# Kernel tuning notes

Hardware: AMD Instinct MI355X
Metric: run time of the kernel (lower is better)

The kernel has to match this reference:

```python
import jax, jax.numpy as jnp
import numpy as np

B, T, C = 2, 2048, 768
H, N_LEFT = 12, 6
D = C // H


def setup_inputs() -> dict:
    key = jax.random.key(0)
    ks = jax.random.split(key, 4)
    x = jax.random.normal(ks[0], (B, T, C), dtype=jnp.float32)
    attention_mask = jnp.ones((B, T), dtype=jnp.int32)
    Wqkv_w = jax.random.normal(ks[1], (3 * C, C), dtype=jnp.float32) * (C ** -0.5)
    Wqkv_b = jnp.zeros((3 * C,), dtype=jnp.float32)
    Wo_w = jax.random.normal(ks[2], (C, C), dtype=jnp.float32) * (C ** -0.5)
    Wo_b = jnp.zeros((C,), dtype=jnp.float32)
    return {"x": x, "attention_mask": attention_mask, "Wqkv_w": Wqkv_w,
            "Wqkv_b": Wqkv_b, "Wo_w": Wo_w, "Wo_b": Wo_b}


def _attend(q, k, v, mask):
    # q,k,v: [B,h,T,D]; mask: [B,1,T,T] additive
    s = jnp.einsum('bhqd,bhkd->bhqk', q, k) * (D ** -0.5) + mask
    a = jax.nn.softmax(s.astype(jnp.float32), axis=-1).astype(q.dtype)
    return jnp.einsum('bhqk,bhkd->bhqd', a, v)


def reference(x, attention_mask, Wqkv_w, Wqkv_b, Wo_w, Wo_b):
    neg = jnp.finfo(x.dtype).min
    # padding mask [B,1,1,T]: 0 where valid, neg where padded
    pad = (1.0 - attention_mask.astype(x.dtype))[:, None, None, :] * neg
    i = jnp.arange(T)
    tri = (i[None, :] > i[:, None]).astype(x.dtype) * neg   # triu(neg, 1)
    left_mask = tri[None, None] + pad                        # causal (look left)
    right_mask = tri.T[None, None] + pad                     # anti-causal (look right)

    qkv = (x @ Wqkv_w.T + Wqkv_b).reshape(B, T, 3, H, D)
    qkv = jnp.transpose(qkv, (0, 3, 2, 1, 4))                # [B,H,3,T,D]
    q, k, v = qkv[:, :, 0], qkv[:, :, 1], qkv[:, :, 2]

    lc = _attend(q[:, :N_LEFT], k[:, :N_LEFT], v[:, :N_LEFT], left_mask)
    rc = _attend(q[:, N_LEFT:], k[:, N_LEFT:], v[:, N_LEFT:], right_mask)
    ctx = jnp.concatenate([lc, rc], axis=1)                  # [B,H,T,D]
    ctx = jnp.transpose(ctx, (0, 2, 1, 3)).reshape(B, T, C)
    out = ctx @ Wo_w.T + Wo_b
    return out
```

## Files before the change

kernel.cpp:

```cpp
#include <hip/hip_runtime.h>


typedef unsigned short u16;
typedef __bf16 bf16x8 __attribute__((ext_vector_type(8)));
typedef float fx4 __attribute__((ext_vector_type(4)));
typedef unsigned short u16x8 __attribute__((ext_vector_type(8)));
typedef unsigned short u16x4 __attribute__((ext_vector_type(4)));
typedef _Float16 hx4 __attribute__((ext_vector_type(4)));
typedef __fp16 fp16x2 __attribute__((ext_vector_type(2)));

#define T_SEQ 2048
#define C_DIM 768
#define NHEAD 12
#define HDIM  64
#define NITEMS 768
#define LOG2E_8 0.18033688f

__device__ __forceinline__ u16 f2bf(float f) {
  unsigned u = __float_as_uint(f);
  u += 0x7fffu + ((u >> 16) & 1u);
  return (u16)(u >> 16);
}
__device__ __forceinline__ u16 f2h(float f) {
  union { _Float16 h; u16 u; } cv; cv.h = (_Float16)f; return cv.u;
}

__device__ __forceinline__ void gl2lds16(const u16* g, u16* l) {
  __builtin_amdgcn_global_load_lds(
      (const __attribute__((address_space(1))) void*)g,
      (__attribute__((address_space(3))) void*)l, 16, 0, 0);
}

__global__ void cvt_swz_k(const float* __restrict__ in, u16* __restrict__ out, int n8) {
  int i = blockIdx.x * blockDim.x + threadIdx.x;
  if (i >= n8) return;
  const fx4* p = (const fx4*)in + (size_t)i * 2;
  fx4 a = p[0], b = p[1];
  u16x8 o;
  #pragma unroll
  for (int j = 0; j < 4; ++j) { o[j] = f2bf(a[j]); o[4 + j] = f2bf(b[j]); }
  int m = i / 96;
  int c8 = (i - m * 96) << 3;
  *(u16x8*)&out[(size_t)m * C_DIM + (c8 ^ ((m & 7) << 3))] = o;
}

__global__ void maskcvt_k(const int* __restrict__ am, float* __restrict__ mf, int n) {
  int i = blockIdx.x * blockDim.x + threadIdx.x;
  if (i < n) mf[i] = am[i] ? 0.f : -1e30f;
}

__device__ __forceinline__ void gemm_core128(const u16* __restrict__ A,
                                             const u16* __restrict__ B,
                                             int m0, int n0,
                                             u16* As, u16* Bs,
                                             fx4 acc[4][4]) {
  const int tid = threadIdx.x;
  const int lane = tid & 63, wv = tid >> 6;
  const int wm = (wv & 1) << 6, wn = (wv >> 1) << 6;
  const int lr = lane & 15, lg = lane >> 4;
  const int swk = (lr & 7) << 3;
  const int srow = (wv << 3) + (lane >> 3);
  const int scol = (lane & 7) << 3;
  #pragma unroll
  for (int mt = 0; mt < 4; ++mt)
    #pragma unroll
    for (int nt = 0; nt < 4; ++nt) acc[mt][nt] = fx4{0.f, 0.f, 0.f, 0.f};

  #pragma unroll
  for (int p = 0; p < 4; ++p) {
    int row = srow + (p << 5);
    gl2lds16(&A[(size_t)(m0 + row) * C_DIM + scol], &As[(row << 6) + scol]);
    gl2lds16(&B[(size_t)(n0 + row) * C_DIM + scol], &Bs[(row << 6) + scol]);
  }

  int buf = 0;
  for (int k0 = 0; k0 < C_DIM; k0 += 64, buf ^= 1) {
    __syncthreads();
    if (k0 + 64 < C_DIM) {
      u16* Ad = &As[(buf ^ 1) << 13];
      u16* Bd = &Bs[(buf ^ 1) << 13];
      #pragma unroll
      for (int p = 0; p < 4; ++p) {
        int row = srow + (p << 5);
        gl2lds16(&A[(size_t)(m0 + row) * C_DIM + k0 + 64 + scol], &Ad[(row << 6) + scol]);
        gl2lds16(&B[(size_t)(n0 + row) * C_DIM + k0 + 64 + scol], &Bd[(row << 6) + scol]);
      }
    }
    const u16* Ab = &As[buf << 13];
    const u16* Bb = &Bs[buf << 13];
    #pragma unroll
    for (int kk = 0; kk < 64; kk += 32) {
      bf16x8 af[4], bfr[4];
      #pragma unroll
      for (int mt = 0; mt < 4; ++mt)
        af[mt] = *(const bf16x8*)&Ab[((wm + mt * 16 + lr) << 6) + ((kk + lg * 8) ^ swk)];
      #pragma unroll
      for (int nt = 0; nt < 4; ++nt)
        bfr[nt] = *(const bf16x8*)&Bb[((wn + nt * 16 + lr) << 6) + ((kk + lg * 8) ^ swk)];
      #pragma unroll
      for (int mt = 0; mt < 4; ++mt)
        #pragma unroll
        for (int nt = 0; nt < 4; ++nt)
          acc[mt][nt] = __builtin_amdgcn_mfma_f32_16x16x32_bf16(
              af[mt], bfr[nt], acc[mt][nt], 0, 0, 0);
    }
  }
}

__global__ __launch_bounds__(256) void gemm_qkv_k(
    const u16* __restrict__ A, const u16* __restrict__ B,
    const float* __restrict__ bias,
    u16* __restrict__ qb, u16* __restrict__ kswz, u16* __restrict__ vswz) {
  __shared__ __align__(16) u16 As[2][128 * 64];
  __shared__ __align__(16) u16 Bs[2][128 * 64];
  int m0 = blockIdx.y << 7, n0 = blockIdx.x << 7;
  fx4 acc[4][4];
  gemm_core128(A, B, m0, n0, &As[0][0], &Bs[0][0], acc);

  const int tid = threadIdx.x, lane = tid & 63, wv = tid >> 6;
  const int wm = (wv & 1) << 6, wn = (wv >> 1) << 6;
  const int lr = lane & 15, lg = lane >> 4;
  #pragma unroll
  for (int nt = 0; nt < 4; ++nt) {
    int n = n0 + wn + nt * 16 + lr;
    float bv = bias[n];
    int part = n / 768;
    int rem = n - part * 768;
    int h = rem >> 6, d = rem & 63;
    #pragma unroll
    for (int mt = 0; mt < 4; ++mt) {
      #pragma unroll
      for (int r = 0; r < 4; ++r) {
        int m = m0 + wm + mt * 16 + lg * 4 + r;
        int bb = m >> 11, t = m & 2047;
        int bh = bb * NHEAD + h;
        int kt = t >> 6, tr = t & 63;
        float val = acc[mt][nt][r] + bv;
        if (part == 0) {
          qb[(((size_t)bh << 11) + t) * HDIM + d] = f2bf(val);
        } else if (part == 1) {
          kswz[((size_t)(bh * 32 + kt) << 12) + (tr << 6) + (d ^ ((tr & 7) << 3))] =
              f2bf(val);
        } else {
          vswz[((size_t)(bh * 32 + kt) << 12) + (d << 6) + (tr ^ ((d & 15) << 2))] =
              f2h(val);
        }
      }
    }
  }
}

__device__ __forceinline__ void gemm_core64(const u16* __restrict__ A,
                                            const u16* __restrict__ B,
                                            int m0, int n0,
                                            u16* As, u16* Bs,
                                            fx4 acc[4][2]) {
  const int tid = threadIdx.x;
  const int lane = tid & 63, wv = tid >> 6;
  const int wn = wv << 5;
  const int lr = lane & 15, lg = lane >> 4;
  const int swk = (lr & 7) << 3;
  const int srow = (wv << 3) + (lane >> 3);
  const int scol = (lane & 7) << 3;
  #pragma unroll
  for (int mt = 0; mt < 4; ++mt)
    #pragma unroll
    for (int nt = 0; nt < 2; ++nt) acc[mt][nt] = fx4{0.f, 0.f, 0.f, 0.f};

  #pragma unroll
  for (int p = 0; p < 2; ++p) {
    int row = srow + (p << 5);
    gl2lds16(&A[(size_t)(m0 + row) * C_DIM + scol], &As[(row << 6) + scol]);
  }
  #pragma unroll
  for (int p = 0; p < 4; ++p) {
    int row = srow + (p << 5);
    gl2lds16(&B[(size_t)(n0 + row) * C_DIM + scol], &Bs[(row << 6) + scol]);
  }

  int buf = 0;
  for (int k0 = 0; k0 < C_DIM; k0 += 64, buf ^= 1) {
    __syncthreads();
    if (k0 + 64 < C_DIM) {
      u16* Ad = &As[(buf ^ 1) << 12];
      u16* Bd = &Bs[(buf ^ 1) << 13];
      #pragma unroll
      for (int p = 0; p < 2; ++p) {
        int row = srow + (p << 5);
        gl2lds16(&A[(size_t)(m0 + row) * C_DIM + k0 + 64 + scol], &Ad[(row << 6) + scol]);
      }
      #pragma unroll
      for (int p = 0; p < 4; ++p) {
        int row = srow + (p << 5);
        gl2lds16(&B[(size_t)(n0 + row) * C_DIM + k0 + 64 + scol], &Bd[(row << 6) + scol]);
      }
    }
    const u16* Ab = &As[buf << 12];
    const u16* Bb = &Bs[buf << 13];
    #pragma unroll
    for (int kk = 0; kk < 64; kk += 32) {
      bf16x8 af[4], bfr[2];
      #pragma unroll
      for (int mt = 0; mt < 4; ++mt)
        af[mt] = *(const bf16x8*)&Ab[((mt * 16 + lr) << 6) + ((kk + lg * 8) ^ swk)];
      #pragma unroll
      for (int nt = 0; nt < 2; ++nt)
        bfr[nt] = *(const bf16x8*)&Bb[((wn + nt * 16 + lr) << 6) + ((kk + lg * 8) ^ swk)];
      #pragma unroll
      for (int mt = 0; mt < 4; ++mt)
        #pragma unroll
        for (int nt = 0; nt < 2; ++nt)
          acc[mt][nt] = __builtin_amdgcn_mfma_f32_16x16x32_bf16(
              af[mt], bfr[nt], acc[mt][nt], 0, 0, 0);
    }
  }
}

__global__ __launch_bounds__(256) void gemm_out_k(
    const u16* __restrict__ A, const u16* __restrict__ B,
    const float* __restrict__ bias, float* __restrict__ out) {
  __shared__ __align__(16) u16 As[2][64 * 64];
  __shared__ __align__(16) u16 Bs[2][128 * 64];
  int m0 = blockIdx.y << 6, n0 = blockIdx.x << 7;
  fx4 acc[4][2];
  gemm_core64(A, B, m0, n0, &As[0][0], &Bs[0][0], acc);

  const int tid = threadIdx.x, lane = tid & 63, wv = tid >> 6;
  const int wn = wv << 5;
  const int lr = lane & 15, lg = lane >> 4;
  #pragma unroll
  for (int nt = 0; nt < 2; ++nt) {
    int n = n0 + wn + nt * 16 + lr;
    float bv = bias[n];
    #pragma unroll
    for (int mt = 0; mt < 4; ++mt) {
      #pragma unroll
      for (int r = 0; r < 4; ++r) {
        int m = m0 + mt * 16 + lg * 4 + r;
        out[(size_t)m * C_DIM + n] = acc[mt][nt][r] + bv;
      }
    }
  }
}

__global__ __launch_bounds__(256) void attn_k(
    const u16* __restrict__ q, const u16* __restrict__ kswz,
    const u16* __restrict__ vswz, const float* __restrict__ maskf,
    u16* __restrict__ ctx, int* __restrict__ counter) {
  __shared__ __align__(16) u16 Ks[2][4096];
  __shared__ __align__(16) u16 Vt[2][4096];
  __shared__ int s_w;

  const int tid = threadIdx.x, lane = tid & 63, wv = tid >> 6;
  const int lr = lane & 15, lg = lane >> 4;
  const int swk = (lr & 7) << 3;
  const int swv = (lr & 15) << 2;

  for (;;) {
    if (tid == 0) s_w = atomicAdd(counter, 1);
    __syncthreads();
    int w = s_w;
    if (w >= NITEMS) break;
    int qslot = w / 24, bh = w - qslot * 24;
    int bb = bh / NHEAD, h = bh - bb * NHEAD;
    bool causal = (h < 6);
    int qt = causal ? (31 - qslot) : qslot;
    int kt0 = causal ? 0 : qt;
    int kt1 = causal ? qt : 31;
    size_t tile_base = (size_t)(bh * 32) << 12;

    {
      const u16* kg = kswz + tile_base + ((size_t)kt0 << 12);
      const u16* vg = vswz + tile_base + ((size_t)kt0 << 12);
      #pragma unroll
      for (int c2 = 0; c2 < 2; ++c2) {
        int e = (wv << 10) + (c2 << 9) + (lane << 3);
        gl2lds16(kg + e, &Ks[0][e]);
        gl2lds16(vg + e, &Vt[0][e]);
      }
    }

    int q0 = qt << 6;
    size_t head_off = ((size_t)bh << 11) * HDIM;
    int qrow = q0 + wv * 16 + lr;
    bf16x8 qf0 = *(const bf16x8*)&q[head_off + (size_t)qrow * HDIM + lg * 8];
    bf16x8 qf1 = *(const bf16x8*)&q[head_off + (size_t)qrow * HDIM + 32 + lg * 8];
    const float* mrow = maskf + (bb << 11);

    fx4 o[4];
    #pragma unroll
    for (int dt = 0; dt < 4; ++dt) o[dt] = fx4{0.f, 0.f, 0.f, 0.f};
    float l_i = 0.f;

    int buf = 0;
    for (int kt = kt0; kt <= kt1; ++kt, buf ^= 1) {
      __syncthreads();
      if (kt < kt1) {
        const u16* kg = kswz + tile_base + ((size_t)(kt + 1) << 12);
        const u16* vg = vswz + tile_base + ((size_t)(kt + 1) << 12);
        #pragma unroll
        for (int c2 = 0; c2 < 2; ++c2) {
          int e = (wv << 10) + (c2 << 9) + (lane << 3);
          gl2lds16(kg + e, &Ks[buf ^ 1][e]);
          gl2lds16(vg + e, &Vt[buf ^ 1][e]);
        }
      }

      fx4 st[4];
      #pragma unroll
      for (int nt = 0; nt < 4; ++nt) {
        const u16* kr = &Ks[buf][(nt * 16 + lr) << 6];
        bf16x8 kf0 = *(const bf16x8*)&kr[(lg * 8) ^ swk];
        bf16x8 kf1 = *(const bf16x8*)&kr[(32 + lg * 8) ^ swk];
        fx4 z = fx4{0.f, 0.f, 0.f, 0.f};
        z = __builtin_amdgcn_mfma_f32_16x16x32_bf16(kf0, qf0, z, 0, 0, 0);
        st[nt] = __builtin_amdgcn_mfma_f32_16x16x32_bf16(kf1, qf1, z, 0, 0, 0);
      }

      const bool diag = (kt == qt);
      float psum = 0.f;
      #pragma unroll
      for (int nt = 0; nt < 4; ++nt) {
        int kb0 = (kt << 6) + nt * 16 + lg * 4;
        fx4 mv = *(const fx4*)&mrow[kb0];
        #pragma unroll
        for (int r = 0; r < 4; ++r) {
          float arg = st[nt][r] * LOG2E_8 + mv[r];
          if (diag) {
            int kabs = kb0 + r;
            bool dead = causal ? (kabs > qrow) : (kabs < qrow);
            arg = dead ? -1e30f : arg;
          }
          float p = __builtin_amdgcn_exp2f(arg);
          st[nt][r] = p;
          psum += p;
        }
      }
      l_i += psum;

      #pragma unroll
      for (int nt = 0; nt < 4; ++nt) {
        union { hx4 v; fp16x2 h[2]; } pu;
        pu.h[0] = __builtin_amdgcn_cvt_pkrtz(st[nt][0], st[nt][1]);
        pu.h[1] = __builtin_amdgcn_cvt_pkrtz(st[nt][2], st[nt][3]);
        hx4 pf = pu.v;
        #pragma unroll
        for (int dt = 0; dt < 4; ++dt) {
          const u16* vr = &Vt[buf][(dt * 16 + lr) << 6];
          hx4 vf = *(const hx4*)&vr[(nt * 16 + lg * 4) ^ swv];
          o[dt] = __builtin_amdgcn_mfma_f32_16x16x16f16(vf, pf, o[dt], 0, 0, 0);
        }
      }
    }

    l_i += __shfl_xor(l_i, 16, 64);
    l_i += __shfl_xor(l_i, 32, 64);
    float inv = 1.f / l_i;
    size_t rowb = ((size_t)(bb << 11) + qrow) * C_DIM;
    int csw = (qrow & 7) << 3;
    #pragma unroll
    for (int dt = 0; dt < 4; ++dt) {
      u16x4 pk;
      #pragma unroll
      for (int r = 0; r < 4; ++r) pk[r] = f2bf(o[dt][r] * inv);
      int colb = h * HDIM + dt * 16 + lg * 4;
      *(u16x4*)&ctx[rowb + (colb ^ csw)] = pk;
    }
  }
}

extern "C" void kernel_launch(void* const* d_in, const int* in_sizes, int n_in,
                              void* d_out, int out_size, void* d_ws, size_t ws_size,
                              hipStream_t stream) {
  const float* x     = (const float*)d_in[0];
  const int*   amask = (const int*)d_in[1];
  const float* wqkv  = (const float*)d_in[2];
  const float* bqkv  = (const float*)d_in[3];
  const float* wo    = (const float*)d_in[4];
  const float* bo    = (const float*)d_in[5];
  float* out = (float*)d_out;

  char* ws = (char*)d_ws;
  u16*   xb    = (u16*)(ws + 0);
  u16*   wqkvb = (u16*)(ws + 6291456);
  u16*   wob   = (u16*)(ws + 9830400);
  u16*   qb    = (u16*)(ws + 11010048);
  u16*   kswz  = (u16*)(ws + 17301504);
  u16*   vswz  = (u16*)(ws + 23592960);
  u16*   ctxb  = (u16*)(ws + 29884416);
  float* maskf = (float*)(ws + 36175872);
  int*   cnt   = (int*)(ws + 36192256);

  cvt_swz_k<<<(393216 + 255) / 256, 256, 0, stream>>>(x, xb, 393216);
  cvt_swz_k<<<(221184 + 255) / 256, 256, 0, stream>>>(wqkv, wqkvb, 221184);
  cvt_swz_k<<<(73728 + 255) / 256, 256, 0, stream>>>(wo, wob, 73728);
  maskcvt_k<<<16, 256, 0, stream>>>(amask, maskf, 4096);
  (void)hipMemsetAsync(cnt, 0, 4, stream);

  gemm_qkv_k<<<dim3(18, 32), 256, 0, stream>>>(xb, wqkvb, bqkv, qb, kswz, vswz);
  attn_k<<<512, 256, 0, stream>>>(qb, kswz, vswz, maskf, ctxb, cnt);
  gemm_out_k<<<dim3(6, 64), 256, 0, stream>>>(ctxb, wob, bo, out);
}
```

Before: 189.4 us.

## Merge conversion launches, shrink GEMM K-tile to 32, raise attention grid size

The three fp32-to-bf16 conversion launches become one kernel that picks its source tensor by row index. It relies on the workspace buffers for x, Wqkv and Wo being contiguous. Both GEMM cores now stage 32-wide K tiles instead of 64, with a new LDS swizzle that keeps the global source layout intact. This halves shared memory per block but doubles the number of barriers per GEMM. The attention launch grows from 512 to 640 blocks, presumably to improve occupancy or load balance through its atomic work counter.

After: 207.0 us. +9.3%, slower.

```diff
diff --git a/kernel.cpp b/kernel.cpp
--- a/kernel.cpp
+++ b/kernel.cpp
@@ -31,16 +31,22 @@
       (__attribute__((address_space(3))) void*)l, 16, 0, 0);
 }
 
-__global__ void cvt_swz_k(const float* __restrict__ in, u16* __restrict__ out, int n8) {
+__global__ void cvt_swz_k(const float* __restrict__ x,
+                          const float* __restrict__ wqkv,
+                          const float* __restrict__ wo,
+                          u16* __restrict__ out) {
   int i = blockIdx.x * blockDim.x + threadIdx.x;
-  if (i >= n8) return;
-  const fx4* p = (const fx4*)in + (size_t)i * 2;
-  fx4 a = p[0], b = p[1];
-  u16x8 o;
-  #pragma unroll
-  for (int j = 0; j < 4; ++j) { o[j] = f2bf(a[j]); o[4 + j] = f2bf(b[j]); }
+  if (i >= 688128) return;
   int m = i / 96;
   int c8 = (i - m * 96) << 3;
+  const float* src;
+  if (m < 4096)       src = x    + (size_t)m * C_DIM + c8;
+  else if (m < 6400)  src = wqkv + (size_t)(m - 4096) * C_DIM + c8;
+  else                src = wo   + (size_t)(m - 6400) * C_DIM + c8;
+  fx4 a = *(const fx4*)src, b = *(const fx4*)(src + 4);
+  u16x8 o;
+  #pragma unroll
+  for (int j = 0; j < 4; ++j) { o[j] = f2bf(a[j]); o[4 + j] = f2bf(b[j]); }
   *(u16x8*)&out[(size_t)m * C_DIM + (c8 ^ ((m & 7) << 3))] = o;
 }
 
@@ -58,52 +64,60 @@
   const int lane = tid & 63, wv = tid >> 6;
   const int wm = (wv & 1) << 6, wn = (wv >> 1) << 6;
   const int lr = lane & 15, lg = lane >> 4;
-  const int swk = (lr & 7) << 3;
-  const int srow = (wv << 3) + (lane >> 3);
-  const int scol = (lane & 7) << 3;
   #pragma unroll
   for (int mt = 0; mt < 4; ++mt)
     #pragma unroll
     for (int nt = 0; nt < 4; ++nt) acc[mt][nt] = fx4{0.f, 0.f, 0.f, 0.f};
 
-  #pragma unroll
-  for (int p = 0; p < 4; ++p) {
-    int row = srow + (p << 5);
-    gl2lds16(&A[(size_t)(m0 + row) * C_DIM + scol], &As[(row << 6) + scol]);
-    gl2lds16(&B[(size_t)(n0 + row) * C_DIM + scol], &Bs[(row << 6) + scol]);
+  int srow[2], sgc[2];
+  #pragma unroll
+  for (int p = 0; p < 2; ++p) {
+    int c = tid + (p << 8);
+    srow[p] = c >> 2;
+    sgc[p] = c & 3;
+  }
+
+  #pragma unroll
+  for (int p = 0; p < 2; ++p) {
+    int row = srow[p];
+    int gcol = ((sgc[p] ^ (row & 3)) << 3) ^ ((row & 7) << 3);
+    gl2lds16(&A[(size_t)(m0 + row) * C_DIM + gcol], &As[(tid + (p << 8)) << 3]);
+    gl2lds16(&B[(size_t)(n0 + row) * C_DIM + gcol], &Bs[(tid + (p << 8)) << 3]);
   }
 
   int buf = 0;
-  for (int k0 = 0; k0 < C_DIM; k0 += 64, buf ^= 1) {
+  for (int k0 = 0; k0 < C_DIM; k0 += 32, buf ^= 1) {
     __syncthreads();
-    if (k0 + 64 < C_DIM) {
-      u16* Ad = &As[(buf ^ 1) << 13];
-      u16* Bd = &Bs[(buf ^ 1) << 13];
-      #pragma unroll
-      for (int p = 0; p < 4; ++p) {
-        int row = srow + (p << 5);
-        gl2lds16(&A[(size_t)(m0 + row) * C_DIM + k0 + 64 + scol], &Ad[(row << 6) + scol]);
-        gl2lds16(&B[(size_t)(n0 + row) * C_DIM + k0 + 64 + scol], &Bd[(row << 6) + scol]);
-      }
-    }
-    const u16* Ab = &As[buf << 13];
-    const u16* Bb = &Bs[buf << 13];
-    #pragma unroll
-    for (int kk = 0; kk < 64; kk += 32) {
-      bf16x8 af[4], bfr[4];
-      #pragma unroll
-      for (int mt = 0; mt < 4; ++mt)
-        af[mt] = *(const bf16x8*)&Ab[((wm + mt * 16 + lr) << 6) + ((kk + lg * 8) ^ swk)];
+    if (k0 + 32 < C_DIM) {
+      u16* Ad = &As[(buf ^ 1) << 12];
+      u16* Bd = &Bs[(buf ^ 1) << 12];
+      #pragma unroll
+      for (int p = 0; p < 2; ++p) {
+        int row = srow[p];
+        int gcol = (k0 + 32 + ((sgc[p] ^ (row & 3)) << 3)) ^ ((row & 7) << 3);
+        gl2lds16(&A[(size_t)(m0 + row) * C_DIM + gcol], &Ad[(tid + (p << 8)) << 3]);
+        gl2lds16(&B[(size_t)(n0 + row) * C_DIM + gcol], &Bd[(tid + (p << 8)) << 3]);
+      }
+    }
+    const u16* Ab = &As[buf << 12];
+    const u16* Bb = &Bs[buf << 12];
+    bf16x8 af[4], bfr[4];
+    #pragma unroll
+    for (int mt = 0; mt < 4; ++mt) {
+      int R = wm + mt * 16 + lr;
+      af[mt] = *(const bf16x8*)&Ab[(R << 5) + ((lg ^ (R & 3)) << 3)];
+    }
+    #pragma unroll
+    for (int nt = 0; nt < 4; ++nt) {
+      int R = wn + nt * 16 + lr;
+      bfr[nt] = *(const bf16x8*)&Bb[(R << 5) + ((lg ^ (R & 3)) << 3)];
+    }
+    #pragma unroll
+    for (int mt = 0; mt < 4; ++mt)
       #pragma unroll
       for (int nt = 0; nt < 4; ++nt)
-        bfr[nt] = *(const bf16x8*)&Bb[((wn + nt * 16 + lr) << 6) + ((kk + lg * 8) ^ swk)];
-      #pragma unroll
-      for (int mt = 0; mt < 4; ++mt)
-        #pragma unroll
-        for (int nt = 0; nt < 4; ++nt)
-          acc[mt][nt] = __builtin_amdgcn_mfma_f32_16x16x32_bf16(
-              af[mt], bfr[nt], acc[mt][nt], 0, 0, 0);
-    }
+        acc[mt][nt] = __builtin_amdgcn_mfma_f32_16x16x32_bf16(
+            af[mt], bfr[nt], acc[mt][nt], 0, 0, 0);
   }
 }
 
@@ -111,8 +125,8 @@
     const u16* __restrict__ A, const u16* __restrict__ B,
     const float* __restrict__ bias,
     u16* __restrict__ qb, u16* __restrict__ kswz, u16* __restrict__ vswz) {
-  __shared__ __align__(16) u16 As[2][128 * 64];
-  __shared__ __align__(16) u16 Bs[2][128 * 64];
+  __shared__ __align__(16) u16 As[2][128 * 32];
+  __shared__ __align__(16) u16 Bs[2][128 * 32];
   int m0 = blockIdx.y << 7, n0 = blockIdx.x << 7;
   fx4 acc[4][4];
   gemm_core128(A, B, m0, n0, &As[0][0], &Bs[0][0], acc);
@@ -159,68 +173,72 @@
   const int lane = tid & 63, wv = tid >> 6;
   const int wn = wv << 5;
   const int lr = lane & 15, lg = lane >> 4;
-  const int swk = (lr & 7) << 3;
-  const int srow = (wv << 3) + (lane >> 3);
-  const int scol = (lane & 7) << 3;
   #pragma unroll
   for (int mt = 0; mt < 4; ++mt)
     #pragma unroll
     for (int nt = 0; nt < 2; ++nt) acc[mt][nt] = fx4{0.f, 0.f, 0.f, 0.f};
 
+  int arow = tid >> 2, ac8 = tid & 3;
+  int brow[2], bc8[2];
   #pragma unroll
   for (int p = 0; p < 2; ++p) {
-    int row = srow + (p << 5);
-    gl2lds16(&A[(size_t)(m0 + row) * C_DIM + scol], &As[(row << 6) + scol]);
-  }
-  #pragma unroll
-  for (int p = 0; p < 4; ++p) {
-    int row = srow + (p << 5);
-    gl2lds16(&B[(size_t)(n0 + row) * C_DIM + scol], &Bs[(row << 6) + scol]);
+    int c = tid + (p << 8);
+    brow[p] = c >> 2; bc8[p] = c & 3;
+  }
+
+  {
+    int gcolA = ((ac8 ^ (arow & 3)) << 3) ^ ((arow & 7) << 3);
+    gl2lds16(&A[(size_t)(m0 + arow) * C_DIM + gcolA], &As[tid << 3]);
+    #pragma unroll
+    for (int p = 0; p < 2; ++p) {
+      int row = brow[p];
+      int gcol = ((bc8[p] ^ (row & 3)) << 3) ^ ((row & 7) << 3);
+      gl2lds16(&B[(size_t)(n0 + row) * C_DIM + gcol], &Bs[(tid + (p << 8)) << 3]);
+    }
   }
 
   int buf = 0;
-  for (int k0 = 0; k0 < C_DIM; k0 += 64, buf ^= 1) {
+  for (int k0 = 0; k0 < C_DIM; k0 += 32, buf ^= 1) {
     __syncthreads();
-    if (k0 + 64 < C_DIM) {
-      u16* Ad = &As[(buf ^ 1) << 12];
-      u16* Bd = &Bs[(buf ^ 1) << 13];
+    if (k0 + 32 < C_DIM) {
+      u16* Ad = &As[(buf ^ 1) << 11];
+      u16* Bd = &Bs[(buf ^ 1) << 12];
+      int gcolA = (k0 + 32 + ((ac8 ^ (arow & 3)) << 3)) ^ ((arow & 7) << 3);
+      gl2lds16(&A[(size_t)(m0 + arow) * C_DIM + gcolA], &Ad[tid << 3]);
       #pragma unroll
       for (int p = 0; p < 2; ++p) {
-        int row = srow + (p << 5);
-        gl2lds16(&A[(size_t)(m0 + row) * C_DIM + k0 + 64 + scol], &Ad[(row << 6) + scol]);
-      }
-      #pragma unroll
-      for (int p = 0; p < 4; ++p) {
-        int row = srow + (p << 5);
-        gl2lds16(&B[(size_t)(n0 + row) * C_DIM + k0 + 64 + scol], &Bd[(row << 6) + scol]);
-      }
-    }
-    const u16* Ab = &As[buf << 12];
-    const u16* Bb = &Bs[buf << 13];
-    #pragma unroll
-    for (int kk = 0; kk < 64; kk += 32) {
-      bf16x8 af[4], bfr[2];
-      #pragma unroll
-      for (int mt = 0; mt < 4; ++mt)
-        af[mt] = *(const bf16x8*)&Ab[((mt * 16 + lr) << 6) + ((kk + lg * 8) ^ swk)];
+        int row = brow[p];
+        int gcol = (k0 + 32 + ((bc8[p] ^ (row & 3)) << 3)) ^ ((row & 7) << 3);
+        gl2lds16(&B[(size_t)(n0 + row) * C_DIM + gcol], &Bd[(tid + (p << 8)) << 3]);
+      }
+    }
+    const u16* Ab = &As[buf << 11];
+    const u16* Bb = &Bs[buf << 12];
+    bf16x8 af[4], bfr[2];
+    #pragma unroll
+    for (int mt = 0; mt < 4; ++mt) {
+      int R = mt * 16 + lr;
+      af[mt] = *(const bf16x8*)&Ab[(R << 5) + ((lg ^ (R & 3)) << 3)];
+    }
+    #pragma unroll
+    for (int nt = 0; nt < 2; ++nt) {
+      int R = wn + nt * 16 + lr;
+      bfr[nt] = *(const bf16x8*)&Bb[(R << 5) + ((lg ^ (R & 3)) << 3)];
+    }
+    #pragma unroll
+    for (int mt = 0; mt < 4; ++mt)
       #pragma unroll
       for (int nt = 0; nt < 2; ++nt)
-        bfr[nt] = *(const bf16x8*)&Bb[((wn + nt * 16 + lr) << 6) + ((kk + lg * 8) ^ swk)];
-      #pragma unroll
-      for (int mt = 0; mt < 4; ++mt)
-        #pragma unroll
-        for (int nt = 0; nt < 2; ++nt)
-          acc[mt][nt] = __builtin_amdgcn_mfma_f32_16x16x32_bf16(
-              af[mt], bfr[nt], acc[mt][nt], 0, 0, 0);
-    }
+        acc[mt][nt] = __builtin_amdgcn_mfma_f32_16x16x32_bf16(
+            af[mt], bfr[nt], acc[mt][nt], 0, 0, 0);
   }
 }
 
 __global__ __launch_bounds__(256) void gemm_out_k(
     const u16* __restrict__ A, const u16* __restrict__ B,
     const float* __restrict__ bias, float* __restrict__ out) {
-  __shared__ __align__(16) u16 As[2][64 * 64];
-  __shared__ __align__(16) u16 Bs[2][128 * 64];
+  __shared__ __align__(16) u16 As[2][64 * 32];
+  __shared__ __align__(16) u16 Bs[2][128 * 32];
   int m0 = blockIdx.y << 6, n0 = blockIdx.x << 7;
   fx4 acc[4][2];
   gemm_core64(A, B, m0, n0, &As[0][0], &Bs[0][0], acc);
@@ -391,13 +409,11 @@
   float* maskf = (float*)(ws + 36175872);
   int*   cnt   = (int*)(ws + 36192256);
 
-  cvt_swz_k<<<(393216 + 255) / 256, 256, 0, stream>>>(x, xb, 393216);
-  cvt_swz_k<<<(221184 + 255) / 256, 256, 0, stream>>>(wqkv, wqkvb, 221184);
-  cvt_swz_k<<<(73728 + 255) / 256, 256, 0, stream>>>(wo, wob, 73728);
+  cvt_swz_k<<<2688, 256, 0, stream>>>(x, wqkv, wo, xb);
   maskcvt_k<<<16, 256, 0, stream>>>(amask, maskf, 4096);
   (void)hipMemsetAsync(cnt, 0, 4, stream);
 
   gemm_qkv_k<<<dim3(18, 32), 256, 0, stream>>>(xb, wqkvb, bqkv, qb, kswz, vswz);
-  attn_k<<<512, 256, 0, stream>>>(qb, kswz, vswz, maskf, ctxb, cnt);
+  attn_k<<<640, 256, 0, stream>>>(qb, kswz, vswz, maskf, ctxb, cnt);
   gemm_out_k<<<dim3(6, 64), 256, 0, stream>>>(ctxb, wob, bo, out);
 }
```

## Merge conversion launches, shrink GEMM tiles, split diagonal softmax path

Applied to the files above, without the earlier changes.

Combines the three fp32-to-bf16 conversion kernels into a single launch writing into the contiguous workspace. The QKV GEMM moves to 64x128 tiles and the output GEMM to 64x64 tiles, with single-buffered LDS loads and two barriers per k-step, raising block count for better CU occupancy. The attention softmax hoists the diagonal-tile check out of the inner loop so off-diagonal tiles skip masking logic. Dropping double buffering may expose global load latency.

Measured after the change: 170.7 us. -9.9%, faster.

```diff
diff --git a/kernel.cpp b/kernel.cpp
--- a/kernel.cpp
+++ b/kernel.cpp
@@ -31,16 +31,22 @@
       (__attribute__((address_space(3))) void*)l, 16, 0, 0);
 }
 
-__global__ void cvt_swz_k(const float* __restrict__ in, u16* __restrict__ out, int n8) {
+__global__ void cvt_swz_k(const float* __restrict__ x,
+                          const float* __restrict__ wqkv,
+                          const float* __restrict__ wo,
+                          u16* __restrict__ out) {
   int i = blockIdx.x * blockDim.x + threadIdx.x;
-  if (i >= n8) return;
-  const fx4* p = (const fx4*)in + (size_t)i * 2;
-  fx4 a = p[0], b = p[1];
-  u16x8 o;
-  #pragma unroll
-  for (int j = 0; j < 4; ++j) { o[j] = f2bf(a[j]); o[4 + j] = f2bf(b[j]); }
+  if (i >= 688128) return;
   int m = i / 96;
   int c8 = (i - m * 96) << 3;
+  const float* src;
+  if (m < 4096)       src = x    + (size_t)m * C_DIM + c8;
+  else if (m < 6400)  src = wqkv + (size_t)(m - 4096) * C_DIM + c8;
+  else                src = wo   + (size_t)(m - 6400) * C_DIM + c8;
+  fx4 a = *(const fx4*)src, b = *(const fx4*)(src + 4);
+  u16x8 o;
+  #pragma unroll
+  for (int j = 0; j < 4; ++j) { o[j] = f2bf(a[j]); o[4 + j] = f2bf(b[j]); }
   *(u16x8*)&out[(size_t)m * C_DIM + (c8 ^ ((m & 7) << 3))] = o;
 }
 
@@ -49,58 +55,48 @@
   if (i < n) mf[i] = am[i] ? 0.f : -1e30f;
 }
 
-__device__ __forceinline__ void gemm_core128(const u16* __restrict__ A,
-                                             const u16* __restrict__ B,
-                                             int m0, int n0,
-                                             u16* As, u16* Bs,
-                                             fx4 acc[4][4]) {
+__device__ __forceinline__ void gemm_core_64x128(const u16* __restrict__ A,
+                                                 const u16* __restrict__ B,
+                                                 int m0, int n0,
+                                                 u16* As, u16* Bs,
+                                                 fx4 acc[4][2]) {
   const int tid = threadIdx.x;
   const int lane = tid & 63, wv = tid >> 6;
-  const int wm = (wv & 1) << 6, wn = (wv >> 1) << 6;
+  const int wn = wv << 5;
   const int lr = lane & 15, lg = lane >> 4;
   const int swk = (lr & 7) << 3;
-  const int srow = (wv << 3) + (lane >> 3);
-  const int scol = (lane & 7) << 3;
+  const int scol = (tid & 7) << 3;
   #pragma unroll
   for (int mt = 0; mt < 4; ++mt)
     #pragma unroll
-    for (int nt = 0; nt < 4; ++nt) acc[mt][nt] = fx4{0.f, 0.f, 0.f, 0.f};
-
-  #pragma unroll
-  for (int p = 0; p < 4; ++p) {
-    int row = srow + (p << 5);
-    gl2lds16(&A[(size_t)(m0 + row) * C_DIM + scol], &As[(row << 6) + scol]);
-    gl2lds16(&B[(size_t)(n0 + row) * C_DIM + scol], &Bs[(row << 6) + scol]);
-  }
-
-  int buf = 0;
-  for (int k0 = 0; k0 < C_DIM; k0 += 64, buf ^= 1) {
-    __syncthreads();
-    if (k0 + 64 < C_DIM) {
-      u16* Ad = &As[(buf ^ 1) << 13];
-      u16* Bd = &Bs[(buf ^ 1) << 13];
-      #pragma unroll
-      for (int p = 0; p < 4; ++p) {
-        int row = srow + (p << 5);
-        gl2lds16(&A[(size_t)(m0 + row) * C_DIM + k0 + 64 + scol], &Ad[(row << 6) + scol]);
-        gl2lds16(&B[(size_t)(n0 + row) * C_DIM + k0 + 64 + scol], &Bd[(row << 6) + scol]);
-      }
-    }
-    const u16* Ab = &As[buf << 13];
-    const u16* Bb = &Bs[buf << 13];
+    for (int nt = 0; nt < 2; ++nt) acc[mt][nt] = fx4{0.f, 0.f, 0.f, 0.f};
+
+  for (int k0 = 0; k0 < C_DIM; k0 += 64) {
+    __syncthreads();
+    #pragma unroll
+    for (int p = 0; p < 2; ++p) {
+      int row = (tid + (p << 8)) >> 3;
+      gl2lds16(&A[(size_t)(m0 + row) * C_DIM + k0 + scol], &As[(row << 6) + scol]);
+    }
+    #pragma unroll
+    for (int p = 0; p < 4; ++p) {
+      int row = (tid + (p << 8)) >> 3;
+      gl2lds16(&B[(size_t)(n0 + row) * C_DIM + k0 + scol], &Bs[(row << 6) + scol]);
+    }
+    __syncthreads();
     #pragma unroll
     for (int kk = 0; kk < 64; kk += 32) {
-      bf16x8 af[4], bfr[4];
+      bf16x8 af[4], bfr[2];
       #pragma unroll
       for (int mt = 0; mt < 4; ++mt)
-        af[mt] = *(const bf16x8*)&Ab[((wm + mt * 16 + lr) << 6) + ((kk + lg * 8) ^ swk)];
-      #pragma unroll
-      for (int nt = 0; nt < 4; ++nt)
-        bfr[nt] = *(const bf16x8*)&Bb[((wn + nt * 16 + lr) << 6) + ((kk + lg * 8) ^ swk)];
+        af[mt] = *(const bf16x8*)&As[((mt * 16 + lr) << 6) + ((kk + lg * 8) ^ swk)];
+      #pragma unroll
+      for (int nt = 0; nt < 2; ++nt)
+        bfr[nt] = *(const bf16x8*)&Bs[((wn + nt * 16 + lr) << 6) + ((kk + lg * 8) ^ swk)];
       #pragma unroll
       for (int mt = 0; mt < 4; ++mt)
         #pragma unroll
-        for (int nt = 0; nt < 4; ++nt)
+        for (int nt = 0; nt < 2; ++nt)
           acc[mt][nt] = __builtin_amdgcn_mfma_f32_16x16x32_bf16(
               af[mt], bfr[nt], acc[mt][nt], 0, 0, 0);
     }
@@ -111,17 +107,17 @@
     const u16* __restrict__ A, const u16* __restrict__ B,
     const float* __restrict__ bias,
     u16* __restrict__ qb, u16* __restrict__ kswz, u16* __restrict__ vswz) {
-  __shared__ __align__(16) u16 As[2][128 * 64];
-  __shared__ __align__(16) u16 Bs[2][128 * 64];
-  int m0 = blockIdx.y << 7, n0 = blockIdx.x << 7;
-  fx4 acc[4][4];
-  gemm_core128(A, B, m0, n0, &As[0][0], &Bs[0][0], acc);
+  __shared__ __align__(16) u16 As[64 * 64];
+  __shared__ __align__(16) u16 Bs[128 * 64];
+  int m0 = blockIdx.y << 6, n0 = blockIdx.x << 7;
+  fx4 acc[4][2];
+  gemm_core_64x128(A, B, m0, n0, As, Bs, acc);
 
   const int tid = threadIdx.x, lane = tid & 63, wv = tid >> 6;
-  const int wm = (wv & 1) << 6, wn = (wv >> 1) << 6;
-  const int lr = lane & 15, lg = lane >> 4;
-  #pragma unroll
-  for (int nt = 0; nt < 4; ++nt) {
+  const int wn = wv << 5;
+  const int lr = lane & 15, lg = lane >> 4;
+  #pragma unroll
+  for (int nt = 0; nt < 2; ++nt) {
     int n = n0 + wn + nt * 16 + lr;
     float bv = bias[n];
     int part = n / 768;
@@ -131,7 +127,7 @@
     for (int mt = 0; mt < 4; ++mt) {
       #pragma unroll
       for (int r = 0; r < 4; ++r) {
-        int m = m0 + wm + mt * 16 + lg * 4 + r;
+        int m = m0 + mt * 16 + lg * 4 + r;
         int bb = m >> 11, t = m & 2047;
         int bh = bb * NHEAD + h;
         int kt = t >> 6, tr = t & 63;
@@ -150,64 +146,42 @@
   }
 }
 
-__device__ __forceinline__ void gemm_core64(const u16* __restrict__ A,
-                                            const u16* __restrict__ B,
-                                            int m0, int n0,
-                                            u16* As, u16* Bs,
-                                            fx4 acc[4][2]) {
+__device__ __forceinline__ void gemm_core_64x64(const u16* __restrict__ A,
+                                                const u16* __restrict__ B,
+                                                int m0, int n0,
+                                                u16* As, u16* Bs,
+                                                fx4 acc[2][2]) {
   const int tid = threadIdx.x;
   const int lane = tid & 63, wv = tid >> 6;
-  const int wn = wv << 5;
+  const int wm = (wv & 1) << 5, wn = (wv >> 1) << 5;
   const int lr = lane & 15, lg = lane >> 4;
   const int swk = (lr & 7) << 3;
-  const int srow = (wv << 3) + (lane >> 3);
-  const int scol = (lane & 7) << 3;
-  #pragma unroll
-  for (int mt = 0; mt < 4; ++mt)
+  const int scol = (tid & 7) << 3;
+  #pragma unroll
+  for (int mt = 0; mt < 2; ++mt)
     #pragma unroll
     for (int nt = 0; nt < 2; ++nt) acc[mt][nt] = fx4{0.f, 0.f, 0.f, 0.f};
 
-  #pragma unroll
-  for (int p = 0; p < 2; ++p) {
-    int row = srow + (p << 5);
-    gl2lds16(&A[(size_t)(m0 + row) * C_DIM + scol], &As[(row << 6) + scol]);
-  }
-  #pragma unroll
-  for (int p = 0; p < 4; ++p) {
-    int row = srow + (p << 5);
-    gl2lds16(&B[(size_t)(n0 + row) * C_DIM + scol], &Bs[(row << 6) + scol]);
-  }
-
-  int buf = 0;
-  for (int k0 = 0; k0 < C_DIM; k0 += 64, buf ^= 1) {
-    __syncthreads();
-    if (k0 + 64 < C_DIM) {
-      u16* Ad = &As[(buf ^ 1) << 12];
-      u16* Bd = &Bs[(buf ^ 1) << 13];
-      #pragma unroll
-      for (int p = 0; p < 2; ++p) {
-        int row = srow + (p << 5);
-        gl2lds16(&A[(size_t)(m0 + row) * C_DIM + k0 + 64 + scol], &Ad[(row << 6) + scol]);
-      }
-      #pragma unroll
-      for (int p = 0; p < 4; ++p) {
-        int row = srow + (p << 5);
-        gl2lds16(&B[(size_t)(n0 + row) * C_DIM + k0 + 64 + scol], &Bd[(row << 6) + scol]);
-      }
-    }
-    const u16* Ab = &As[buf << 12];
-    const u16* Bb = &Bs[buf << 13];
+  for (int k0 = 0; k0 < C_DIM; k0 += 64) {
+    __syncthreads();
+    #pragma unroll
+    for (int p = 0; p < 2; ++p) {
+      int row = (tid + (p << 8)) >> 3;
+      gl2lds16(&A[(size_t)(m0 + row) * C_DIM + k0 + scol], &As[(row << 6) + scol]);
+      gl2lds16(&B[(size_t)(n0 + row) * C_DIM + k0 + scol], &Bs[(row << 6) + scol]);
+    }
+    __syncthreads();
     #pragma unroll
     for (int kk = 0; kk < 64; kk += 32) {
-      bf16x8 af[4], bfr[2];
-      #pragma unroll
-      for (int mt = 0; mt < 4; ++mt)
-        af[mt] = *(const bf16x8*)&Ab[((mt * 16 + lr) << 6) + ((kk + lg * 8) ^ swk)];
+      bf16x8 af[2], bfr[2];
+      #pragma unroll
+      for (int mt = 0; mt < 2; ++mt)
+        af[mt] = *(const bf16x8*)&As[((wm + mt * 16 + lr) << 6) + ((kk + lg * 8) ^ swk)];
       #pragma unroll
       for (int nt = 0; nt < 2; ++nt)
-        bfr[nt] = *(const bf16x8*)&Bb[((wn + nt * 16 + lr) << 6) + ((kk + lg * 8) ^ swk)];
-      #pragma unroll
-      for (int mt = 0; mt < 4; ++mt)
+        bfr[nt] = *(const bf16x8*)&Bs[((wn + nt * 16 + lr) << 6) + ((kk + lg * 8) ^ swk)];
+      #pragma unroll
+      for (int mt = 0; mt < 2; ++mt)
         #pragma unroll
         for (int nt = 0; nt < 2; ++nt)
           acc[mt][nt] = __builtin_amdgcn_mfma_f32_16x16x32_bf16(
@@ -219,24 +193,24 @@
 __global__ __launch_bounds__(256) void gemm_out_k(
     const u16* __restrict__ A, const u16* __restrict__ B,
     const float* __restrict__ bias, float* __restrict__ out) {
-  __shared__ __align__(16) u16 As[2][64 * 64];
-  __shared__ __align__(16) u16 Bs[2][128 * 64];
-  int m0 = blockIdx.y << 6, n0 = blockIdx.x << 7;
-  fx4 acc[4][2];
-  gemm_core64(A, B, m0, n0, &As[0][0], &Bs[0][0], acc);
+  __shared__ __align__(16) u16 As[64 * 64];
+  __shared__ __align__(16) u16 Bs[64 * 64];
+  int m0 = blockIdx.y << 6, n0 = blockIdx.x << 6;
+  fx4 acc[2][2];
+  gemm_core_64x64(A, B, m0, n0, As, Bs, acc);
 
   const int tid = threadIdx.x, lane = tid & 63, wv = tid >> 6;
-  const int wn = wv << 5;
+  const int wm = (wv & 1) << 5, wn = (wv >> 1) << 5;
   const int lr = lane & 15, lg = lane >> 4;
   #pragma unroll
   for (int nt = 0; nt < 2; ++nt) {
     int n = n0 + wn + nt * 16 + lr;
     float bv = bias[n];
     #pragma unroll
-    for (int mt = 0; mt < 4; ++mt) {
+    for (int mt = 0; mt < 2; ++mt) {
       #pragma unroll
       for (int r = 0; r < 4; ++r) {
-        int m = m0 + mt * 16 + lg * 4 + r;
+        int m = m0 + wm + mt * 16 + lg * 4 + r;
         out[(size_t)m * C_DIM + n] = acc[mt][nt][r] + bv;
       }
     }
@@ -317,23 +291,34 @@
         st[nt] = __builtin_amdgcn_mfma_f32_16x16x32_bf16(kf1, qf1, z, 0, 0, 0);
       }
 
-      const bool diag = (kt == qt);
       float psum = 0.f;
-      #pragma unroll
-      for (int nt = 0; nt < 4; ++nt) {
-        int kb0 = (kt << 6) + nt * 16 + lg * 4;
-        fx4 mv = *(const fx4*)&mrow[kb0];
-        #pragma unroll
-        for (int r = 0; r < 4; ++r) {
-          float arg = st[nt][r] * LOG2E_8 + mv[r];
-          if (diag) {
+      if (kt == qt) {
+        #pragma unroll
+        for (int nt = 0; nt < 4; ++nt) {
+          int kb0 = (kt << 6) + nt * 16 + lg * 4;
+          fx4 mv = *(const fx4*)&mrow[kb0];
+          #pragma unroll
+          for (int r = 0; r < 4; ++r) {
+            float arg = st[nt][r] * LOG2E_8 + mv[r];
             int kabs = kb0 + r;
             bool dead = causal ? (kabs > qrow) : (kabs < qrow);
             arg = dead ? -1e30f : arg;
+            float p = __builtin_amdgcn_exp2f(arg);
+            st[nt][r] = p;
+            psum += p;
           }
-          float p = __builtin_amdgcn_exp2f(arg);
-          st[nt][r] = p;
-          psum += p;
+        }
+      } else {
+        #pragma unroll
+        for (int nt = 0; nt < 4; ++nt) {
+          int kb0 = (kt << 6) + nt * 16 + lg * 4;
+          fx4 mv = *(const fx4*)&mrow[kb0];
+          #pragma unroll
+          for (int r = 0; r < 4; ++r) {
+            float p = __builtin_amdgcn_exp2f(st[nt][r] * LOG2E_8 + mv[r]);
+            st[nt][r] = p;
+            psum += p;
+          }
         }
       }
       l_i += psum;
@@ -391,13 +376,11 @@
   float* maskf = (float*)(ws + 36175872);
   int*   cnt   = (int*)(ws + 36192256);
 
-  cvt_swz_k<<<(393216 + 255) / 256, 256, 0, stream>>>(x, xb, 393216);
-  cvt_swz_k<<<(221184 + 255) / 256, 256, 0, stream>>>(wqkv, wqkvb, 221184);
-  cvt_swz_k<<<(73728 + 255) / 256, 256, 0, stream>>>(wo, wob, 73728);
+  cvt_swz_k<<<2688, 256, 0, stream>>>(x, wqkv, wo, xb);
   maskcvt_k<<<16, 256, 0, stream>>>(amask, maskf, 4096);
   (void)hipMemsetAsync(cnt, 0, 4, stream);
 
-  gemm_qkv_k<<<dim3(18, 32), 256, 0, stream>>>(xb, wqkvb, bqkv, qb, kswz, vswz);
+  gemm_qkv_k<<<dim3(18, 64), 256, 0, stream>>>(xb, wqkvb, bqkv, qb, kswz, vswz);
   attn_k<<<512, 256, 0, stream>>>(qb, kswz, vswz, maskf, ctxb, cnt);
-  gemm_out_k<<<dim3(6, 64), 256, 0, stream>>>(ctxb, wob, bo, out);
-}
+  gemm_out_k<<<dim3(12, 64), 256, 0, stream>>>(ctxb, wob, bo, out);
+}
```
